# Performance work log

Measured on AMD Instinct MI355X. Metric: run time of the kernel, lower is better.

Reference implementation:

```python
import jax, jax.numpy as jnp
import numpy as np

DIM = 1024

def setup_inputs() -> dict:
    key = jax.random.key(0)
    ks = jax.random.split(key, 8)
    B, Sx, Sy, D = 4, 2048, 2048, DIM
    s = 1.0 / np.sqrt(D)
    return {
        "x": jax.random.normal(ks[0], (B, Sx, D), jnp.float32),
        "y": jax.random.normal(ks[1], (B, Sy, D), jnp.float32),
        "Wq": jax.random.normal(ks[2], (D, D), jnp.float32) * s,
        "bq": jnp.zeros((D,), jnp.float32),
        "Wk": jax.random.normal(ks[3], (D, D), jnp.float32) * s,
        "bk": jnp.zeros((D,), jnp.float32),
        "Wv": jax.random.normal(ks[4], (D, D), jnp.float32) * s,
        "bv": jnp.zeros((D,), jnp.float32),
    }

def reference(x, y, Wq, bq, Wk, bk, Wv, bv):
    D = x.shape[-1]
    scale = jnp.sqrt(jnp.asarray(D, x.dtype))
    Q = jnp.einsum('bsd,de->bse', x, Wq) + bq  # [B,Sx,D]
    K = jnp.einsum('btd,de->bte', y, Wk) + bk  # [B,Sy,D]
    V = jnp.einsum('btd,de->bte', y, Wv) + bv  # [B,Sy,D]
    scores = jnp.einsum('bse,bte->bst', Q, K) / scale  # [B,Sx,Sy]
    probs = jax.nn.softmax(scores, axis=-1)
    out = jnp.einsum('bst,bte->bse', probs, V)  # [B,Sx,D]
    return out
```

## Files before the change

kernel.cpp:

```cpp
#include <hip/hip_runtime.h>

typedef __bf16 bf16x8_t __attribute__((ext_vector_type(8)));
typedef float f32x4_t __attribute__((ext_vector_type(4)));
typedef unsigned short ushort_t;

__device__ __forceinline__ unsigned short f2bf(float f) {
  unsigned u = __float_as_uint(f);
  u = (u + 0x7FFFu + ((u >> 16) & 1u)) >> 16;
  return (unsigned short)u;
}
__device__ __forceinline__ float bf2f(unsigned short h) {
  return __uint_as_float(((unsigned)h) << 16);
}

__device__ __forceinline__ void gload16(const void* g, void* l) {
  __builtin_amdgcn_global_load_lds(
      (const __attribute__((address_space(1))) unsigned int*)g,
      (__attribute__((address_space(3))) unsigned int*)l, 16, 0, 0);
}

template<bool OUT_BF16, bool HAS_BIAS>
__global__ __launch_bounds__(256, 3)
void gemm_nt(const ushort_t* __restrict__ A, const ushort_t* __restrict__ Bt,
             void* __restrict__ Cp, const float* __restrict__ bias,
             int gx, int gy, int K, int lda, int ldb, int ldc,
             long sA, long sB, long sC, float alpha)
{
  __shared__ __align__(16) ushort_t smem[2][8192];
  const int tid = threadIdx.x;
  const int lane = tid & 63;
  const int wave = tid >> 6;

  const int per = gridDim.x >> 3;
  int wg = blockIdx.x;
  wg = (wg & 7) * per + (wg >> 3);
  const int bz = wg / (gx * gy);
  const int rr = wg - bz * gx * gy;
  const int by = rr / gx, bx = rr - by * gx;
  const int bm = by * 128, bn = bx * 128;

  const ushort_t* Ab = A + (long)bz * sA;
  const ushort_t* Bb = Bt + (long)bz * sB;

  const int r_s0 = wave * 16 + (lane >> 2);
  const int r_s1 = (wave + 4) * 16 + (lane >> 2);
  const int c_s0 = (((lane & 3) ^ ((r_s0 >> 1) & 3)) << 3);
  const int c_s1 = (((lane & 3) ^ ((r_s1 >> 1) & 3)) << 3);
  const ushort_t* gA0 = Ab + (long)(bm + r_s0) * lda + c_s0;
  const ushort_t* gA1 = Ab + (long)(bm + r_s1) * lda + c_s1;
  const ushort_t* gB0 = Bb + (long)(bn + r_s0) * ldb + c_s0;
  const ushort_t* gB1 = Bb + (long)(bn + r_s1) * ldb + c_s1;

  auto stage = [&](int kt, int buf) {
    const int k0 = kt << 5;
    ushort_t* s = smem[buf];
    gload16(gA0 + k0, s + wave * 512);
    gload16(gA1 + k0, s + (wave + 4) * 512);
    gload16(gB0 + k0, s + 4096 + wave * 512);
    gload16(gB1 + k0, s + 4096 + (wave + 4) * 512);
  };

  const int wr = wave >> 1, wc = wave & 1;
  int offA[4], offB[4];
#pragma unroll
  for (int m = 0; m < 4; ++m) {
    const int row = wr * 64 + m * 16 + (lane & 15);
    offA[m] = row * 32 + ((((lane >> 4) ^ ((row >> 1) & 3))) << 3);
  }
#pragma unroll
  for (int n = 0; n < 4; ++n) {
    const int row = wc * 64 + n * 16 + (lane & 15);
    offB[n] = 4096 + row * 32 + ((((lane >> 4) ^ ((row >> 1) & 3))) << 3);
  }

  f32x4_t acc[4][4];
  const f32x4_t z4 = {0.f, 0.f, 0.f, 0.f};
#pragma unroll
  for (int m = 0; m < 4; ++m)
#pragma unroll
    for (int n = 0; n < 4; ++n) acc[m][n] = z4;

  stage(0, 0);
  __syncthreads();

  const int nt = K >> 5;
  for (int kt = 0; kt < nt; ++kt) {
    const int cur = kt & 1;
    if (kt + 1 < nt) stage(kt + 1, cur ^ 1);
    const ushort_t* s = smem[cur];
    bf16x8_t af[4], bfv[4];
#pragma unroll
    for (int m = 0; m < 4; ++m)
      af[m] = __builtin_bit_cast(bf16x8_t, *(const uint4*)(s + offA[m]));
#pragma unroll
    for (int n = 0; n < 4; ++n)
      bfv[n] = __builtin_bit_cast(bf16x8_t, *(const uint4*)(s + offB[n]));
#pragma unroll
    for (int m = 0; m < 4; ++m)
#pragma unroll
      for (int n = 0; n < 4; ++n)
        acc[m][n] = __builtin_amdgcn_mfma_f32_16x16x32_bf16(af[m], bfv[n], acc[m][n], 0, 0, 0);
    __syncthreads();
  }

  const long zC = (long)bz * sC;
  const int r0 = (lane >> 4) * 4;
  const int c0 = lane & 15;
#pragma unroll
  for (int m = 0; m < 4; ++m) {
    const int grow0 = bm + wr * 64 + m * 16 + r0;
#pragma unroll
    for (int n = 0; n < 4; ++n) {
      const int gcol = bn + wc * 64 + n * 16 + c0;
      float bv_ = 0.f;
      if constexpr (HAS_BIAS) bv_ = bias[gcol];
#pragma unroll
      for (int i = 0; i < 4; ++i) {
        const float v = acc[m][n][i] * alpha + bv_;
        if constexpr (OUT_BF16) {
          ((ushort_t*)Cp)[zC + (long)(grow0 + i) * ldc + gcol] = f2bf(v);
        } else {
          ((float*)Cp)[zC + (long)(grow0 + i) * ldc + gcol] = v;
        }
      }
    }
  }
}

__global__ __launch_bounds__(256)
void conv_f32_bf16(const float* __restrict__ in, ushort_t* __restrict__ out) {
  const long i = (long)blockIdx.x * 256 + threadIdx.x;
  const float4 a = ((const float4*)in)[i * 2];
  const float4 b = ((const float4*)in)[i * 2 + 1];
  uint4 o;
  o.x = (unsigned)f2bf(a.x) | ((unsigned)f2bf(a.y) << 16);
  o.y = (unsigned)f2bf(a.z) | ((unsigned)f2bf(a.w) << 16);
  o.z = (unsigned)f2bf(b.x) | ((unsigned)f2bf(b.y) << 16);
  o.w = (unsigned)f2bf(b.z) | ((unsigned)f2bf(b.w) << 16);
  ((uint4*)out)[i] = o;
}

__global__ __launch_bounds__(256)
void wtrans(const float* __restrict__ W, ushort_t* __restrict__ Wt) {
  __shared__ float tile[32][33];
  const int bx = blockIdx.x * 32;
  const int by = blockIdx.y * 32;
  const int t = threadIdx.x;
  const int c = t & 31, r0 = t >> 5;
#pragma unroll
  for (int i = 0; i < 4; ++i)
    tile[r0 + i * 8][c] = W[(long)(by + r0 + i * 8) * 1024 + bx + c];
  __syncthreads();
#pragma unroll
  for (int i = 0; i < 4; ++i)
    Wt[(long)(bx + r0 + i * 8) * 1024 + by + c] = f2bf(tile[c][r0 + i * 8]);
}

__global__ __launch_bounds__(256)
void transpose_bf16(const ushort_t* __restrict__ in, ushort_t* __restrict__ out,
                    int rows, int cols) {
  __shared__ ushort_t t[64][65];
  in += (long)blockIdx.z * rows * cols;
  out += (long)blockIdx.z * rows * cols;
  const int r0 = blockIdx.y * 64, c0 = blockIdx.x * 64;
  const int tc = threadIdx.x & 31;
  const int tr = threadIdx.x >> 5;
#pragma unroll
  for (int i = 0; i < 8; ++i) {
    const unsigned v = *(const unsigned*)(in + (long)(r0 + tr + 8 * i) * cols + c0 + tc * 2);
    t[tr + 8 * i][tc * 2] = (ushort_t)(v & 0xffff);
    t[tr + 8 * i][tc * 2 + 1] = (ushort_t)(v >> 16);
  }
  __syncthreads();
#pragma unroll
  for (int i = 0; i < 8; ++i) {
    const unsigned v = (unsigned)t[tc * 2][tr + 8 * i] |
                       ((unsigned)t[tc * 2 + 1][tr + 8 * i] << 16);
    *(unsigned*)(out + (long)(c0 + tr + 8 * i) * rows + r0 + tc * 2) = v;
  }
}

__global__ __launch_bounds__(256)
void softmax_rows(ushort_t* __restrict__ S) {
  const long row = blockIdx.x;
  ushort_t* p = S + row * 2048;
  const int t = threadIdx.x;
  uint4 v = ((uint4*)p)[t];
  ushort_t* hp = (ushort_t*)&v;
  float f[8];
#pragma unroll
  for (int j = 0; j < 8; ++j) f[j] = bf2f(hp[j]);

  float m = f[0];
#pragma unroll
  for (int j = 1; j < 8; ++j) m = fmaxf(m, f[j]);
#pragma unroll
  for (int s = 32; s; s >>= 1) m = fmaxf(m, __shfl_xor(m, s, 64));
  __shared__ float redm[4];
  __shared__ float reds[4];
  const int wave = t >> 6, lane = t & 63;
  if (lane == 0) redm[wave] = m;
  __syncthreads();
  m = fmaxf(fmaxf(redm[0], redm[1]), fmaxf(redm[2], redm[3]));

  float sum = 0.f;
#pragma unroll
  for (int j = 0; j < 8; ++j) { f[j] = __expf(f[j] - m); sum += f[j]; }
#pragma unroll
  for (int s = 32; s; s >>= 1) sum += __shfl_xor(sum, s, 64);
  if (lane == 0) reds[wave] = sum;
  __syncthreads();
  sum = reds[0] + reds[1] + reds[2] + reds[3];
  const float inv = 1.0f / sum;
#pragma unroll
  for (int j = 0; j < 8; ++j) hp[j] = f2bf(f[j] * inv);
  ((uint4*)p)[t] = v;
}

extern "C" void kernel_launch(void* const* d_in, const int* in_sizes, int n_in,
                              void* d_out, int out_size, void* d_ws, size_t ws_size,
                              hipStream_t stream) {
  const float* x  = (const float*)d_in[0];
  const float* y  = (const float*)d_in[1];
  const float* Wq = (const float*)d_in[2];
  const float* bq = (const float*)d_in[3];
  const float* Wk = (const float*)d_in[4];
  const float* bk = (const float*)d_in[5];
  const float* Wv = (const float*)d_in[6];
  const float* bv = (const float*)d_in[7];
  float* out = (float*)d_out;

  const int B = 4, Sx = 2048, Sy = 2048, D = 1024;
  const long M = (long)B * Sx;

  ushort_t* ws  = (ushort_t*)d_ws;
  ushort_t* Wqt = ws;
  ushort_t* Wkt = Wqt + (1u << 20);
  ushort_t* Wvt = Wkt + (1u << 20);
  ushort_t* Qb  = Wvt + (1u << 20);
  ushort_t* Kb  = Qb + (8u << 20);
  ushort_t* Sb  = Kb + (8u << 20);
  ushort_t* xb  = Sb + (16u << 20);
  ushort_t* yb  = xb + (8u << 20);
  ushort_t* Vn  = Sb;
  ushort_t* Vt  = xb;

  dim3 blk(256);

  conv_f32_bf16<<<dim3(4096), blk, 0, stream>>>(x, xb);
  conv_f32_bf16<<<dim3(4096), blk, 0, stream>>>(y, yb);
  wtrans<<<dim3(32, 32), blk, 0, stream>>>(Wq, Wqt);
  wtrans<<<dim3(32, 32), blk, 0, stream>>>(Wk, Wkt);
  wtrans<<<dim3(32, 32), blk, 0, stream>>>(Wv, Wvt);

  gemm_nt<true, true><<<dim3(512), blk, 0, stream>>>(
      xb, Wqt, Qb, bq, 8, 64, D, D, D, D, 0, 0, 0, 1.0f);
  gemm_nt<true, true><<<dim3(512), blk, 0, stream>>>(
      yb, Wkt, Kb, bk, 8, 64, D, D, D, D, 0, 0, 0, 1.0f);
  gemm_nt<true, true><<<dim3(512), blk, 0, stream>>>(
      yb, Wvt, Vn, bv, 8, 64, D, D, D, D, 0, 0, 0, 1.0f);
  transpose_bf16<<<dim3(16, 32, 4), blk, 0, stream>>>(Vn, Vt, Sy, D);

  gemm_nt<true, false><<<dim3(1024), blk, 0, stream>>>(
      Qb, Kb, Sb, nullptr, 16, 16, D, D, D, Sy,
      (long)Sx * D, (long)Sy * D, (long)Sx * Sy, 0.03125f);

  softmax_rows<<<dim3(B * Sx), blk, 0, stream>>>(Sb);

  gemm_nt<false, false><<<dim3(512), blk, 0, stream>>>(
      Sb, Vt, out, nullptr, 8, 16, Sy, Sy, Sy, D,
      (long)Sx * Sy, (long)D * Sy, (long)Sx * D, 1.0f);
}
```

Measured before the change: 208.3 us.

## Add 256x256 ping-pong MFMA GEMM and fuse K/V projections

Adds a new 512-thread GEMM kernel with 256x256 tiles, double-buffered direct-to-LDS loads interleaved across four sub-phases with priority hints, and uses it for the Q, fused K/V, and QK^T GEMMs. K and V projections become one GEMM against concatenated weights (Wk and Wv laid out contiguously) with a concatenated bias, writing an interleaved [K|V] buffer. The transpose takes strided inputs so it can read V from that buffer. Larger tiles cut global traffic and launches, at the cost of fewer workgroups (128–256) on a large-CU device and higher register/LDS pressure.

```diff
diff --git a/kernel.cpp b/kernel.cpp
--- a/kernel.cpp
+++ b/kernel.cpp
@@ -17,6 +17,185 @@
   __builtin_amdgcn_global_load_lds(
       (const __attribute__((address_space(1))) unsigned int*)g,
       (__attribute__((address_space(3))) unsigned int*)l, 16, 0, 0);
+}
+
+#define BARRIER() __builtin_amdgcn_s_barrier()
+#define LGKM0()                                        \
+  do {                                                 \
+    asm volatile("s_waitcnt lgkmcnt(0)" ::: "memory"); \
+    __builtin_amdgcn_sched_barrier(0);                 \
+  } while (0)
+
+template<bool OUT_BF16, bool HAS_BIAS>
+__global__ __launch_bounds__(512, 2)
+void gemm256(const ushort_t* __restrict__ A, const ushort_t* __restrict__ Bt,
+             void* __restrict__ Cp, const float* __restrict__ bias,
+             int gx, int gy, int K, int lda, int ldb, int ldc,
+             long sA, long sB, long sC, float alpha)
+{
+  __shared__ __align__(16) ushort_t sm[2 * 32768];
+  const int tid = threadIdx.x;
+  const int lane = tid & 63;
+  const int w = tid >> 6;
+  const int wr = w >> 2, wc = w & 3;
+
+  const int per = gridDim.x >> 3;
+  int wg = blockIdx.x;
+  wg = (wg & 7) * per + (wg >> 3);
+  const int bz = wg / (gx * gy);
+  const int rr = wg - bz * gx * gy;
+  const int by = rr / gx, bx = rr - by * gx;
+  const int bm = by * 256, bn = bx * 256;
+
+  const int srr = lane >> 3;
+  const int csw = ((lane & 7) ^ srr) << 3;
+  const ushort_t* pA = A + (long)bz * sA + (long)(bm + w * 16 + srr) * lda + csw;
+  const ushort_t* pB = Bt + (long)bz * sB + (long)(bn + w * 16 + srr) * ldb + csw;
+
+  auto stA = [&](int buf, int h, int t) {
+    const ushort_t* g = pA + (long)(h * 128) * lda + t * 64;
+    ushort_t* d = sm + buf * 32768 + h * 8192 + w * 1024;
+    gload16(g, d);
+    gload16(g + 8 * lda, d + 512);
+  };
+  auto stB = [&](int buf, int h, int t) {
+    const ushort_t* g = pB + (long)(h * 128) * ldb + t * 64;
+    ushort_t* d = sm + buf * 32768 + 16384 + h * 8192 + w * 1024;
+    gload16(g, d);
+    gload16(g + 8 * ldb, d + 512);
+  };
+
+  const int q = lane >> 4, x7 = lane & 7;
+  const int cx0 = ((0 + q) ^ x7) << 3;
+  const int cx1 = ((4 + q) ^ x7) << 3;
+  const int abase = wr * 8192 + (lane & 15) * 64;
+  const int bbase = 16384 + wc * 4096 + (lane & 15) * 64;
+
+  f32x4_t acc[8][4];
+  const f32x4_t z4 = {0.f, 0.f, 0.f, 0.f};
+#pragma unroll
+  for (int m = 0; m < 8; ++m)
+#pragma unroll
+    for (int n = 0; n < 4; ++n) acc[m][n] = z4;
+
+  bf16x8_t a[8], blo[4], bhi[4];
+
+  stA(0, 0, 0); stA(0, 1, 0); stB(0, 0, 0); stB(0, 1, 0);
+  stB(1, 0, 1); stB(1, 1, 1); stA(1, 0, 1);
+  asm volatile("s_waitcnt vmcnt(6)" ::: "memory");
+  __builtin_amdgcn_sched_barrier(0);
+  BARRIER();
+
+#define LDX(off) __builtin_bit_cast(bf16x8_t, *(const uint4*)(s + (off)))
+
+  const int nt = K >> 6;
+  for (int t = 0; t < nt; ++t) {
+    const int buf = t & 1;
+    const ushort_t* s = sm + buf * 32768;
+
+#pragma unroll
+    for (int mf = 0; mf < 4; ++mf) {
+      a[mf * 2]     = LDX(abase + mf * 1024 + cx0);
+      a[mf * 2 + 1] = LDX(abase + mf * 1024 + cx1);
+    }
+#pragma unroll
+    for (int nf = 0; nf < 2; ++nf) {
+      blo[nf * 2]     = LDX(bbase + nf * 1024 + cx0);
+      blo[nf * 2 + 1] = LDX(bbase + nf * 1024 + cx1);
+    }
+    if (t + 1 < nt) stA(buf ^ 1, 1, t + 1);
+    BARRIER();
+    LGKM0();
+    __builtin_amdgcn_s_setprio(1);
+#pragma unroll
+    for (int mf = 0; mf < 4; ++mf)
+#pragma unroll
+      for (int nf = 0; nf < 2; ++nf) {
+        acc[mf][nf] = __builtin_amdgcn_mfma_f32_16x16x32_bf16(a[mf * 2], blo[nf * 2], acc[mf][nf], 0, 0, 0);
+        acc[mf][nf] = __builtin_amdgcn_mfma_f32_16x16x32_bf16(a[mf * 2 + 1], blo[nf * 2 + 1], acc[mf][nf], 0, 0, 0);
+      }
+    __builtin_amdgcn_s_setprio(0);
+    BARRIER();
+
+#pragma unroll
+    for (int nf = 0; nf < 2; ++nf) {
+      bhi[nf * 2]     = LDX(bbase + (nf + 2) * 1024 + cx0);
+      bhi[nf * 2 + 1] = LDX(bbase + (nf + 2) * 1024 + cx1);
+    }
+    if (t + 2 < nt) stB(buf, 0, t + 2);
+    BARRIER();
+    LGKM0();
+    __builtin_amdgcn_s_setprio(1);
+#pragma unroll
+    for (int mf = 0; mf < 4; ++mf)
+#pragma unroll
+      for (int nf = 0; nf < 2; ++nf) {
+        acc[mf][nf + 2] = __builtin_amdgcn_mfma_f32_16x16x32_bf16(a[mf * 2], bhi[nf * 2], acc[mf][nf + 2], 0, 0, 0);
+        acc[mf][nf + 2] = __builtin_amdgcn_mfma_f32_16x16x32_bf16(a[mf * 2 + 1], bhi[nf * 2 + 1], acc[mf][nf + 2], 0, 0, 0);
+      }
+    __builtin_amdgcn_s_setprio(0);
+    BARRIER();
+
+#pragma unroll
+    for (int mf = 0; mf < 4; ++mf) {
+      a[mf * 2]     = LDX(abase + (mf + 4) * 1024 + cx0);
+      a[mf * 2 + 1] = LDX(abase + (mf + 4) * 1024 + cx1);
+    }
+    if (t + 2 < nt) stB(buf, 1, t + 2);
+    BARRIER();
+    LGKM0();
+    __builtin_amdgcn_s_setprio(1);
+#pragma unroll
+    for (int mf = 0; mf < 4; ++mf)
+#pragma unroll
+      for (int nf = 0; nf < 2; ++nf) {
+        acc[mf + 4][nf + 2] = __builtin_amdgcn_mfma_f32_16x16x32_bf16(a[mf * 2], bhi[nf * 2], acc[mf + 4][nf + 2], 0, 0, 0);
+        acc[mf + 4][nf + 2] = __builtin_amdgcn_mfma_f32_16x16x32_bf16(a[mf * 2 + 1], bhi[nf * 2 + 1], acc[mf + 4][nf + 2], 0, 0, 0);
+      }
+    __builtin_amdgcn_s_setprio(0);
+    BARRIER();
+
+    if (t + 2 < nt) stA(buf, 0, t + 2);
+    __builtin_amdgcn_s_setprio(1);
+#pragma unroll
+    for (int mf = 0; mf < 4; ++mf)
+#pragma unroll
+      for (int nf = 0; nf < 2; ++nf) {
+        acc[mf + 4][nf] = __builtin_amdgcn_mfma_f32_16x16x32_bf16(a[mf * 2], blo[nf * 2], acc[mf + 4][nf], 0, 0, 0);
+        acc[mf + 4][nf] = __builtin_amdgcn_mfma_f32_16x16x32_bf16(a[mf * 2 + 1], blo[nf * 2 + 1], acc[mf + 4][nf], 0, 0, 0);
+      }
+    __builtin_amdgcn_s_setprio(0);
+    if (t + 1 < nt) {
+      if (t + 2 < nt) asm volatile("s_waitcnt vmcnt(6)" ::: "memory");
+      else            asm volatile("s_waitcnt vmcnt(0)" ::: "memory");
+      __builtin_amdgcn_sched_barrier(0);
+    }
+    BARRIER();
+  }
+#undef LDX
+
+  const long zC = (long)bz * sC;
+  const int r0 = q * 4;
+  const int c0 = lane & 15;
+#pragma unroll
+  for (int mf = 0; mf < 8; ++mf) {
+    const int grow0 = bm + wr * 128 + mf * 16 + r0;
+#pragma unroll
+    for (int nf = 0; nf < 4; ++nf) {
+      const int gcol = bn + wc * 64 + nf * 16 + c0;
+      float bv_ = 0.f;
+      if constexpr (HAS_BIAS) bv_ = bias[gcol];
+#pragma unroll
+      for (int i = 0; i < 4; ++i) {
+        const float v = acc[mf][nf][i] * alpha + bv_;
+        if constexpr (OUT_BF16) {
+          ((ushort_t*)Cp)[zC + (long)(grow0 + i) * ldc + gcol] = f2bf(v);
+        } else {
+          ((float*)Cp)[zC + (long)(grow0 + i) * ldc + gcol] = v;
+        }
+      }
+    }
+  }
 }
 
 template<bool OUT_BF16, bool HAS_BIAS>
@@ -157,26 +336,33 @@
 }
 
 __global__ __launch_bounds__(256)
+void bconcat(const float* __restrict__ a, const float* __restrict__ b,
+             float* __restrict__ o) {
+  const int i = blockIdx.x * 256 + threadIdx.x;
+  o[i] = (i < 1024) ? a[i] : b[i - 1024];
+}
+
+__global__ __launch_bounds__(256)
 void transpose_bf16(const ushort_t* __restrict__ in, ushort_t* __restrict__ out,
-                    int rows, int cols) {
-  __shared__ ushort_t t[64][65];
-  in += (long)blockIdx.z * rows * cols;
-  out += (long)blockIdx.z * rows * cols;
+                    int ld_in, int ld_out, long in_bs, long out_bs) {
+  __shared__ ushort_t tt[64][65];
+  in += (long)blockIdx.z * in_bs;
+  out += (long)blockIdx.z * out_bs;
   const int r0 = blockIdx.y * 64, c0 = blockIdx.x * 64;
   const int tc = threadIdx.x & 31;
   const int tr = threadIdx.x >> 5;
 #pragma unroll
   for (int i = 0; i < 8; ++i) {
-    const unsigned v = *(const unsigned*)(in + (long)(r0 + tr + 8 * i) * cols + c0 + tc * 2);
-    t[tr + 8 * i][tc * 2] = (ushort_t)(v & 0xffff);
-    t[tr + 8 * i][tc * 2 + 1] = (ushort_t)(v >> 16);
+    const unsigned v = *(const unsigned*)(in + (long)(r0 + tr + 8 * i) * ld_in + c0 + tc * 2);
+    tt[tr + 8 * i][tc * 2] = (ushort_t)(v & 0xffff);
+    tt[tr + 8 * i][tc * 2 + 1] = (ushort_t)(v >> 16);
   }
   __syncthreads();
 #pragma unroll
   for (int i = 0; i < 8; ++i) {
-    const unsigned v = (unsigned)t[tc * 2][tr + 8 * i] |
-                       ((unsigned)t[tc * 2 + 1][tr + 8 * i] << 16);
-    *(unsigned*)(out + (long)(c0 + tr + 8 * i) * rows + r0 + tc * 2) = v;
+    const unsigned v = (unsigned)tt[tc * 2][tr + 8 * i] |
+                       ((unsigned)tt[tc * 2 + 1][tr + 8 * i] << 16);
+    *(unsigned*)(out + (long)(c0 + tr + 8 * i) * ld_out + r0 + tc * 2) = v;
   }
 }
 
@@ -230,44 +416,44 @@
   const float* bv = (const float*)d_in[7];
   float* out = (float*)d_out;
 
-  const int B = 4, Sx = 2048, Sy = 2048, D = 1024;
-  const long M = (long)B * Sx;
+  const int D = 1024;
+  const long MB_ = 1l << 20;
 
   ushort_t* ws  = (ushort_t*)d_ws;
   ushort_t* Wqt = ws;
-  ushort_t* Wkt = Wqt + (1u << 20);
-  ushort_t* Wvt = Wkt + (1u << 20);
-  ushort_t* Qb  = Wvt + (1u << 20);
-  ushort_t* Kb  = Qb + (8u << 20);
-  ushort_t* Sb  = Kb + (8u << 20);
-  ushort_t* xb  = Sb + (16u << 20);
-  ushort_t* yb  = xb + (8u << 20);
-  ushort_t* Vn  = Sb;
-  ushort_t* Vt  = xb;
+  ushort_t* Wkv = ws + 1 * MB_;
+  ushort_t* Wvt = ws + 2 * MB_;
+  ushort_t* Qb  = ws + 3 * MB_;
+  ushort_t* KV  = ws + 11 * MB_;
+  ushort_t* yb  = ws + 27 * MB_;
+  ushort_t* Vt  = ws + 27 * MB_;
+  ushort_t* xb  = ws + 35 * MB_;
+  ushort_t* Sb  = ws + 35 * MB_;
+  float*    bkv = (float*)(ws + 51 * MB_);
 
   dim3 blk(256);
 
   conv_f32_bf16<<<dim3(4096), blk, 0, stream>>>(x, xb);
   conv_f32_bf16<<<dim3(4096), blk, 0, stream>>>(y, yb);
   wtrans<<<dim3(32, 32), blk, 0, stream>>>(Wq, Wqt);
-  wtrans<<<dim3(32, 32), blk, 0, stream>>>(Wk, Wkt);
+  wtrans<<<dim3(32, 32), blk, 0, stream>>>(Wk, Wkv);
   wtrans<<<dim3(32, 32), blk, 0, stream>>>(Wv, Wvt);
-
-  gemm_nt<true, true><<<dim3(512), blk, 0, stream>>>(
-      xb, Wqt, Qb, bq, 8, 64, D, D, D, D, 0, 0, 0, 1.0f);
-  gemm_nt<true, true><<<dim3(512), blk, 0, stream>>>(
-      yb, Wkt, Kb, bk, 8, 64, D, D, D, D, 0, 0, 0, 1.0f);
-  gemm_nt<true, true><<<dim3(512), blk, 0, stream>>>(
-      yb, Wvt, Vn, bv, 8, 64, D, D, D, D, 0, 0, 0, 1.0f);
-  transpose_bf16<<<dim3(16, 32, 4), blk, 0, stream>>>(Vn, Vt, Sy, D);
-
-  gemm_nt<true, false><<<dim3(1024), blk, 0, stream>>>(
-      Qb, Kb, Sb, nullptr, 16, 16, D, D, D, Sy,
-      (long)Sx * D, (long)Sy * D, (long)Sx * Sy, 0.03125f);
-
-  softmax_rows<<<dim3(B * Sx), blk, 0, stream>>>(Sb);
+  bconcat<<<dim3(8), blk, 0, stream>>>(bk, bv, bkv);
+
+  gemm256<true, true><<<dim3(128), dim3(512), 0, stream>>>(
+      xb, Wqt, Qb, bq, 4, 32, D, D, D, D, 0, 0, 0, 1.0f);
+  gemm256<true, true><<<dim3(256), dim3(512), 0, stream>>>(
+      yb, Wkv, KV, bkv, 8, 32, D, D, D, 2048, 0, 0, 0, 1.0f);
+  transpose_bf16<<<dim3(16, 32, 4), blk, 0, stream>>>(
+      KV + 1024, Vt, 2048, 2048, 2048l * 2048, 1024l * 2048);
+
+  gemm256<true, false><<<dim3(256), dim3(512), 0, stream>>>(
+      Qb, KV, Sb, nullptr, 8, 8, D, D, 2048, 2048,
+      2048l * 1024, 2048l * 2048, 2048l * 2048, 0.03125f);
+
+  softmax_rows<<<dim3(8192), blk, 0, stream>>>(Sb);
 
   gemm_nt<false, false><<<dim3(512), blk, 0, stream>>>(
-      Sb, Vt, out, nullptr, 8, 16, Sy, Sy, Sy, D,
-      (long)Sx * Sy, (long)D * Sy, (long)Sx * D, 1.0f);
-}
+      Sb, Vt, out, nullptr, 8, 16, 2048, 2048, 2048, D,
+      2048l * 2048, 1024l * 2048, 2048l * 1024, 1.0f);
+}
```

Result: faster. 203.5 us (-2.3%).
